# Performance work log

Measured on AMD Instinct MI355X. Metric: run time of the kernel, lower is better.

The kernel has to match this reference:

```python
import jax, jax.numpy as jnp
import numpy as np

H, DM, LQ, LK, DK, DV = 16, 1024, 2048, 2048, 64, 64
B = 2

def setup_inputs() -> dict:
    key = jax.random.key(0)
    ks = jax.random.split(key, 12)
    s = 0.02  # init scale for weights
    return {
        "Q": jax.random.normal(ks[0], (B, LQ, DM), jnp.float32),
        "K": jax.random.normal(ks[1], (B, LK, DM), jnp.float32),
        "V": jax.random.normal(ks[2], (B, LK, DM), jnp.float32),
        "mask": jax.random.randint(ks[3], (B, LQ), 0, 2, jnp.int32),
        "W_Q": jax.random.normal(ks[4], (H * DK, DM), jnp.float32) * s,
        "b_Q": jnp.zeros((H * DK,), jnp.float32),
        "W_K": jax.random.normal(ks[5], (H * DK, DM), jnp.float32) * s,
        "b_K": jnp.zeros((H * DK,), jnp.float32),
        "W_V": jax.random.normal(ks[6], (H * DV, DM), jnp.float32) * s,
        "b_V": jnp.zeros((H * DV,), jnp.float32),
        "W_O": jax.random.normal(ks[7], (DM, H * DV), jnp.float32) * s,
        "b_O": jnp.zeros((DM,), jnp.float32),
    }

def reference(Q, K, V, mask, W_Q, b_Q, W_K, b_K, W_V, b_V, W_O, b_O):
    b = Q.shape[0]
    q = (Q @ W_Q.T + b_Q).reshape(b, LQ, H, DK)
    k = (K @ W_K.T + b_K).reshape(b, LK, H, DK)
    v = (V @ W_V.T + b_V).reshape(b, LK, H, DV)
    # scores: [b, h, q, k]
    A = jnp.einsum('bqhd,bkhd->bhqk', q, k) / jnp.sqrt(jnp.float32(DK))
    # mask masks whole QUERY rows; softmax is over the query axis (dim=1 in torch's [B*h, lq, lk])
    A = jnp.where(mask[:, None, :, None] == 0, -jnp.inf, A)
    alpha = jax.nn.softmax(A, axis=2)  # over query axis, per original masked branch
    out = jnp.einsum('bhqk,bkhd->bqhd', alpha, v).reshape(b, LQ, H * DV)
    return out @ W_O.T + b_O + Q  # output proj + residual
```

## Files before the change

### kernel.cpp

```cpp
#include <hip/hip_runtime.h>
#include <hip/hip_bf16.h>
#include <stdint.h>

using frag8 = __attribute__((ext_vector_type(8))) short;
using f32x4 = __attribute__((ext_vector_type(4))) float;

#define MFMA16 __builtin_amdgcn_mfma_f32_16x16x32_bf16

#if __has_builtin(__builtin_amdgcn_exp2f)
#define EXP2F(x) __builtin_amdgcn_exp2f(x)
#else
#define EXP2F(x) __expf((x) * 0.6931471805599453f)
#endif
#if __has_builtin(__builtin_amdgcn_rcpf)
#define RCPF(x) __builtin_amdgcn_rcpf(x)
#else
#define RCPF(x) (1.0f / (x))
#endif

#define SCALE_Q 0.18033688011112042f

__device__ __forceinline__ short f2bf(float f) {
    union { __hip_bfloat16 h; short s; } c;
    c.h = __float2bfloat16(f);
    return c.s;
}
__device__ __forceinline__ float bf2f(short s) {
    union { uint32_t u; float f; } x; x.u = ((uint32_t)(uint16_t)s) << 16;
    return x.f;
}
__device__ __forceinline__ uint32_t pack2bf(float a, float b) {
    float2 t; t.x = a; t.y = b;
    __hip_bfloat162 h = __float22bfloat162_rn(t);
    union { __hip_bfloat162 h; uint32_t u; } c; c.h = h;
    return c.u;
}
__device__ __forceinline__ uint32_t addpk(uint32_t a, uint32_t b) {
    float a0 = bf2f((short)(a & 0xffff)), a1 = bf2f((short)(a >> 16));
    float b0 = bf2f((short)(b & 0xffff)), b1 = bf2f((short)(b >> 16));
    return pack2bf(a0 + b0, a1 + b1);
}
__device__ __forceinline__ frag8 add8(uint4 x, uint4 y) {
    union { uint32_t u[4]; frag8 f; } r;
    r.u[0] = addpk(x.x, y.x); r.u[1] = addpk(x.y, y.y);
    r.u[2] = addpk(x.z, y.z); r.u[3] = addpk(x.w, y.w);
    return r.f;
}

__global__ __launch_bounds__(64) void k_compact(const int* __restrict__ mask,
                                                int* __restrict__ idx,
                                                int* __restrict__ invp,
                                                int* __restrict__ nU) {
    const int b = blockIdx.x, ln = threadIdx.x;
    const int* m = mask + b * 2048;
    int tot = 0;
    for (int c = 0; c < 32; c++)
        tot += __popcll(__ballot(m[c * 64 + ln] != 0));
    int base = 0, mbase = tot;
    for (int c = 0; c < 32; c++) {
        int i = c * 64 + ln;
        int mv = m[i];
        unsigned long long bal = __ballot(mv != 0);
        int rank = __popcll(bal & ((1ull << ln) - 1ull));
        int nb = __popcll(bal);
        int pos = mv ? (base + rank) : (mbase + ln - rank);
        invp[b * 2048 + i] = pos;
        if (mv) idx[b * 2048 + pos] = i;
        base += nb; mbase += 64 - nb;
    }
    if (ln == 0) nU[b] = tot;
}

__global__ __launch_bounds__(256) void k_zero2(uint4* __restrict__ a,
                                               uint4* __restrict__ b, int n16) {
    int i = blockIdx.x * 256 + threadIdx.x;
    if (i < n16) { uint4 z = {0, 0, 0, 0}; a[i] = z; b[i] = z; }
}

__global__ __launch_bounds__(256) void k_cvt_all(
    const float* __restrict__ s0, const float* __restrict__ s1,
    const float* __restrict__ s2, const float* __restrict__ s3,
    const float* __restrict__ s4, const float* __restrict__ s5,
    const float* __restrict__ s6,
    short* __restrict__ d0, short* __restrict__ d1, short* __restrict__ d2,
    short* __restrict__ d3, short* __restrict__ d4, short* __restrict__ d5,
    short* __restrict__ d6) {
    const int A4 = 1048576, W4 = 262144;
    int i = blockIdx.x * 256 + threadIdx.x;
    int st = gridDim.x * 256;
    const int total = 3 * A4 + 4 * W4;
    for (; i < total; i += st) {
        const float* s; short* d; int j;
        if (i < A4)            { s = s0; d = d0; j = i; }
        else if (i < 2 * A4)   { s = s1; d = d1; j = i - A4; }
        else if (i < 3 * A4)   { s = s2; d = d2; j = i - 2 * A4; }
        else {
            int t = i - 3 * A4; int seg = t / W4; j = t - seg * W4;
            s = seg == 0 ? s3 : seg == 1 ? s4 : seg == 2 ? s5 : s6;
            d = seg == 0 ? d3 : seg == 1 ? d4 : seg == 2 ? d5 : d6;
        }
        float4 v = reinterpret_cast<const float4*>(s)[j];
        uint2 o;
        o.x = pack2bf(v.x, v.y);
        o.y = pack2bf(v.z, v.w);
        reinterpret_cast<uint2*>(d)[j] = o;
    }
}

__device__ __forceinline__ void stage64x128(const short* __restrict__ g, int rs,
                                            short* lds, int tid) {
#pragma unroll
    for (int j = 0; j < 2; j++) {
        int chunk = j * 256 + tid;
        int row = chunk >> 3, c = chunk & 7;
        int sc = c ^ (row & 7);
        __builtin_amdgcn_global_load_lds(
            (const __attribute__((address_space(1))) uint32_t*)(g + (size_t)row * rs + sc * 8),
            (__attribute__((address_space(3))) uint32_t*)(lds + (j * 256 + (tid & 192)) * 8),
            16, 0, 0);
    }
}
__device__ __forceinline__ frag8 ldswz(const short* lds, int row, int cc) {
    return *(const frag8*)(lds + row * 64 + ((cc ^ (row & 7)) << 3));
}

__device__ __forceinline__ void stage_gswz(const short* __restrict__ g,
                                           short* lds, int tid) {
#pragma unroll
    for (int j = 0; j < 2; j++) {
        int c = j * 256 + tid;
        int lrow = c >> 3;
        int sc = (c & 7) ^ (lrow & 7);
        int grow = lrow * 2 + (sc >> 2);
        int gcol = (sc & 3) * 8;
        __builtin_amdgcn_global_load_lds(
            (const __attribute__((address_space(1))) uint32_t*)(g + (size_t)grow * 1024 + gcol),
            (__attribute__((address_space(3))) uint32_t*)(lds + (j * 256 + (tid & 192)) * 8),
            16, 0, 0);
    }
}
__device__ __forceinline__ frag8 ldgswz(const short* lds, int row, int cc) {
    int lrow = row >> 1;
    int s = (((row & 1) << 2) + cc) ^ (lrow & 7);
    return *(const frag8*)(lds + lrow * 64 + s * 8);
}

__global__ __launch_bounds__(256) void k_proj3(
    const short* __restrict__ A0, const short* __restrict__ A1, const short* __restrict__ A2,
    const short* __restrict__ B0, const short* __restrict__ B1, const short* __restrict__ B2,
    const float* __restrict__ bias0, const float* __restrict__ bias1, const float* __restrict__ bias2,
    const int* __restrict__ invp,
    short* __restrict__ dst0, short* __restrict__ dst1, short* __restrict__ dst2) {
    __shared__ short lA[2][4096];
    __shared__ short lB[2][4096];
    const int wg = blockIdx.x;
    const int tmlow = wg & 7, tnb = (wg >> 3) & 7, rest = wg >> 6;
    const int tmh = rest & 3, z = rest >> 2;
    const int tmb = tmlow | (tmh << 3);
    const short* A  = z == 0 ? A0 : z == 1 ? A1 : A2;
    const short* Bt = z == 0 ? B0 : z == 1 ? B1 : B2;
    const float* bias = z == 0 ? bias0 : z == 1 ? bias1 : bias2;
    short* dst = z == 0 ? dst0 : z == 1 ? dst1 : dst2;
    const float scale = z == 0 ? SCALE_Q : 1.0f;

    const int tid = threadIdx.x, w = tid >> 6, ln = tid & 63;
    const int wm = w >> 1, wn = w & 1, r16 = ln & 15, g = ln >> 4;
    const int tn = tnb * 128, tm = tmb * 128;
    const short* Ab = A + (size_t)tm * 1024;
    const short* Bb = Bt + (size_t)tn * 1024;

    f32x4 acc[4][4] = {};
    stage_gswz(Ab, &lA[0][0], tid);
    stage_gswz(Bb, &lB[0][0], tid);
    int buf = 0;
    for (int ks = 0; ks < 32; ks++) {
        __syncthreads();
        if (ks + 1 < 32) {
            stage_gswz(Ab + (ks + 1) * 32, &lA[buf ^ 1][0], tid);
            stage_gswz(Bb + (ks + 1) * 32, &lB[buf ^ 1][0], tid);
        }
        frag8 af[4], bg[4];
#pragma unroll
        for (int mf = 0; mf < 4; mf++)
            af[mf] = ldgswz(&lA[buf][0], wm * 64 + mf * 16 + r16, g);
#pragma unroll
        for (int nf = 0; nf < 4; nf++)
            bg[nf] = ldgswz(&lB[buf][0], wn * 64 + nf * 16 + r16, g);
#pragma unroll
        for (int mf = 0; mf < 4; mf++)
#pragma unroll
            for (int nf = 0; nf < 4; nf++)
                acc[mf][nf] = MFMA16(af[mf], bg[nf], acc[mf][nf], 0, 0, 0);
        buf ^= 1;
    }
#pragma unroll
    for (int mf = 0; mf < 4; mf++)
#pragma unroll
        for (int r = 0; r < 4; r++) {
            int m = tm + wm * 64 + mf * 16 + g * 4 + r;
            int b = m >> 11, seq = m & 2047;
            int sq = (z == 0) ? invp[b * 2048 + seq] : seq;
#pragma unroll
            for (int nf = 0; nf < 4; nf++) {
                int n = tn + wn * 64 + nf * 16 + r16;
                float val = (acc[mf][nf][r] + bias[n]) * scale;
                int h = n >> 6, d = n & 63;
                dst[((size_t)(b * 16 + h) * 2048 + sq) * 64 + d] = f2bf(val);
            }
        }
}

__global__ __launch_bounds__(256, 3) void k_stats(const short* __restrict__ k_s,
                                                  const short* __restrict__ q_s,
                                                  const int* __restrict__ nU,
                                                  const short* __restrict__ v_s,
                                                  short* __restrict__ vhatT) {
    __shared__ short lQ[2][4096];
    __shared__ float lD[128];
    __shared__ short lT[128 * 70];
    const int wg = blockIdx.x;
    const int x = wg & 7, r2 = wg >> 3;
    const int kt = r2 & 15;
    const int bh = x + 8 * (r2 >> 4);
    const int b = bh >> 4;
    const int n = nU[b], nUr = (n + 63) & ~63;
    const int tid = threadIdx.x, w = tid >> 6, ln = tid & 63;
    const int r16 = ln & 15, g = ln >> 4;
    const int kbase = kt * 128 + w * 32;

    const short* kp = k_s + ((size_t)bh * 2048 + kbase) * 64;
    frag8 kf[2][2];
#pragma unroll
    for (int mfk = 0; mfk < 2; mfk++)
#pragma unroll
        for (int kk = 0; kk < 2; kk++)
            kf[mfk][kk] = *(const frag8*)(kp + (mfk * 16 + r16) * 64 + kk * 32 + g * 8);

    const short* qsp = q_s + (size_t)bh * 2048 * 64;
    float dacc[2][4] = {};
    const f32x4 z4 = {0.f, 0.f, 0.f, 0.f};

    if (nUr > 0) {
        stage64x128(qsp, 64, &lQ[0][0], tid);
        int buf = 0;
        for (int qb = 0; qb < nUr; qb += 64) {
            __syncthreads();
            if (qb + 64 < nUr)
                stage64x128(qsp + (size_t)(qb + 64) * 64, 64, &lQ[buf ^ 1][0], tid);
            const short* Qc = &lQ[buf][0];
#pragma unroll
            for (int nf = 0; nf < 4; nf++) {
                float fm = (qb + nf * 16 + r16 < n) ? 1.0f : 0.0f;
                frag8 bq0 = ldswz(Qc, nf * 16 + r16, g);
                frag8 bq1 = ldswz(Qc, nf * 16 + r16, 4 + g);
#pragma unroll
                for (int mfk = 0; mfk < 2; mfk++) {
                    f32x4 s = MFMA16(kf[mfk][0], bq0, z4, 0, 0, 0);
                    s = MFMA16(kf[mfk][1], bq1, s, 0, 0, 0);
#pragma unroll
                    for (int r = 0; r < 4; r++)
                        dacc[mfk][r] += fm * EXP2F(s[r]);
                }
            }
            buf ^= 1;
        }
    }
#pragma unroll
    for (int mfk = 0; mfk < 2; mfk++)
#pragma unroll
        for (int r = 0; r < 4; r++) {
            float v = dacc[mfk][r];
#pragma unroll
            for (int off = 1; off < 16; off <<= 1)
                v += __shfl_xor(v, off, 16);
            dacc[mfk][r] = v;
        }
    if (r16 == 0) {
#pragma unroll
        for (int mfk = 0; mfk < 2; mfk++)
#pragma unroll
            for (int r = 0; r < 4; r++)
                lD[w * 32 + mfk * 16 + g * 4 + r] = RCPF(dacc[mfk][r]);
    }
    const short* vrow = v_s + ((size_t)bh * 2048 + kt * 128) * 64;
#pragma unroll
    for (int i = 0; i < 8; i++) {
        int idx4 = i * 256 + tid;
        int row = idx4 >> 4, c4 = idx4 & 15;
        uint2 u = *(const uint2*)(vrow + (size_t)row * 64 + c4 * 4);
        *(uint32_t*)&lT[row * 70 + c4 * 4]     = u.x;
        *(uint32_t*)&lT[row * 70 + c4 * 4 + 2] = u.y;
    }
    __syncthreads();
    {
        int d = tid >> 2, kc = tid & 3;
        short* dstp = vhatT + ((size_t)bh * 64 + d) * 2048 + kt * 128 + kc * 32;
        uint32_t wd[16];
#pragma unroll
        for (int j2 = 0; j2 < 16; j2++) {
            int k0 = kc * 32 + j2 * 2;
            float v0 = bf2f(lT[k0 * 70 + d]) * lD[k0];
            float v1 = bf2f(lT[(k0 + 1) * 70 + d]) * lD[k0 + 1];
            wd[j2] = pack2bf(v0, v1);
        }
#pragma unroll
        for (int j4 = 0; j4 < 4; j4++) {
            uint4 o = {wd[j4 * 4], wd[j4 * 4 + 1], wd[j4 * 4 + 2], wd[j4 * 4 + 3]};
            *((uint4*)dstp + j4) = o;
        }
    }
}

__global__ __launch_bounds__(256, 3) void k_apply(const short* __restrict__ q_s,
                                                  const short* __restrict__ k_s,
                                                  const short* __restrict__ vhatT,
                                                  const int* __restrict__ idx,
                                                  const int* __restrict__ nU,
                                                  short* __restrict__ p0,
                                                  short* __restrict__ p1) {
    __shared__ short lK[2][4096];
    __shared__ short lV[2][4096];
    __shared__ short lP[128 * 64];
    const int wg = blockIdx.x;
    const int x = wg & 7, r2 = wg >> 3;
    const int qt = r2 & 15, y = r2 >> 4;
    const int bhsp = (y << 3) | x;
    const int bh = bhsp >> 1, sp = bhsp & 1;
    const int b = bh >> 4, h = bh & 15;
    const int n = nU[b];
    if (qt * 128 >= n) return;
    const int tid = threadIdx.x, w = tid >> 6, ln = tid & 63;
    const int r16 = ln & 15, g = ln >> 4;

    const short* qp = q_s + ((size_t)bh * 2048 + qt * 128 + w * 32) * 64;
    frag8 qf[2][2];
#pragma unroll
    for (int qi = 0; qi < 2; qi++)
#pragma unroll
        for (int kk = 0; kk < 2; kk++)
            qf[qi][kk] = *(const frag8*)(qp + (qi * 16 + r16) * 64 + kk * 32 + g * 8);

    const short* kp = k_s + ((size_t)bh * 2048 + sp * 1024) * 64;
    const short* vp = vhatT + (size_t)bh * 64 * 2048 + sp * 1024;

    f32x4 oacc[2][4] = {};
    const f32x4 z4 = {0.f, 0.f, 0.f, 0.f};

    stage64x128(kp, 64, &lK[0][0], tid);
    stage64x128(vp, 2048, &lV[0][0], tid);
    int buf = 0;
    for (int kb = 0; kb < 1024; kb += 64) {
        __syncthreads();
        if (kb + 64 < 1024) {
            stage64x128(kp + (size_t)(kb + 64) * 64, 64, &lK[buf ^ 1][0], tid);
            stage64x128(vp + kb + 64, 2048, &lV[buf ^ 1][0], tid);
        }
        const short* Kc = &lK[buf][0];
        const short* Vc = &lV[buf][0];
        frag8 vb[4][2];
#pragma unroll
        for (int nf = 0; nf < 4; nf++)
#pragma unroll
            for (int kk = 0; kk < 2; kk++)
                vb[nf][kk] = ldswz(Vc, nf * 16 + r16, kk * 4 + g);
#pragma unroll
        for (int qi = 0; qi < 2; qi++) {
            const int prow = w * 32 + qi * 16 + r16;
            const int rx = prow & 7;
#pragma unroll
            for (int mf2 = 0; mf2 < 4; mf2++) {
                f32x4 s = z4;
#pragma unroll
                for (int kk = 0; kk < 2; kk++)
                    s = MFMA16(ldswz(Kc, mf2 * 16 + r16, kk * 4 + g), qf[qi][kk], s, 0, 0, 0);
                float e0 = EXP2F(s[0]), e1 = EXP2F(s[1]);
                float e2 = EXP2F(s[2]), e3 = EXP2F(s[3]);
                uint2 pk;
                pk.x = pack2bf(e0, e1);
                pk.y = pack2bf(e2, e3);
                int o = mf2 * 32 + g * 8;
                int addr = prow * 128 + (((o >> 4) ^ rx) << 4) + (o & 15);
                *(uint2*)((char*)lP + addr) = pk;
            }
        }
#pragma unroll
        for (int qi = 0; qi < 2; qi++) {
            const int prow = w * 32 + qi * 16 + r16;
            const int rx = prow & 7;
            frag8 pa[2];
#pragma unroll
            for (int kk = 0; kk < 2; kk++)
                pa[kk] = *(const frag8*)((char*)lP + prow * 128 + (((kk * 4 + g) ^ rx) << 4));
#pragma unroll
            for (int nf = 0; nf < 4; nf++)
#pragma unroll
                for (int kk = 0; kk < 2; kk++)
                    oacc[qi][nf] = MFMA16(pa[kk], vb[nf][kk], oacc[qi][nf], 0, 0, 0);
        }
        buf ^= 1;
    }
    short* op = sp ? p1 : p0;
#pragma unroll
    for (int qi = 0; qi < 2; qi++)
#pragma unroll
        for (int r = 0; r < 4; r++) {
            int lq = qt * 128 + w * 32 + qi * 16 + g * 4 + r;
            if (lq < n) {
                int qg = idx[b * 2048 + lq];
#pragma unroll
                for (int nf = 0; nf < 4; nf++) {
                    int d = nf * 16 + r16;
                    op[((size_t)(b * 2048 + qg)) * 1024 + h * 64 + d] = f2bf(oacc[qi][nf][r]);
                }
            }
        }
}

__global__ __launch_bounds__(256) void k_final(const short* __restrict__ p0,
                                               const short* __restrict__ p1,
                                               const short* __restrict__ Bt,
                                               const float* __restrict__ bias,
                                               const float* __restrict__ Qres,
                                               float* __restrict__ out) {
    __shared__ short lA[2][4096];
    __shared__ short lB[2][4096];
    const int wg = blockIdx.x;
    const int tmb = (wg & 7) | ((wg >> 6) << 3);
    const int tnb = (wg >> 3) & 7;
    const int tid = threadIdx.x, w = tid >> 6, ln = tid & 63;
    const int wm = w >> 1, wn = w & 1, r16 = ln & 15, g = ln >> 4;
    const int tn = tnb * 128, tm = tmb * 128;
    const short* A0 = p0 + (size_t)tm * 1024;
    const short* A1 = p1 + (size_t)tm * 1024;
    const short* Bb = Bt + (size_t)tn * 1024;

    const int c0 = (w * 2) * 64 + ln, c1 = c0 + 64;
    const int lr0 = c0 >> 3, s0 = (c0 & 7) ^ (lr0 & 7);
    const int gr0 = lr0 * 2 + (s0 >> 2), gc0 = (s0 & 3) * 8;
    const int lr1 = c1 >> 3, s1 = (c1 & 7) ^ (lr1 & 7);
    const int gr1 = lr1 * 2 + (s1 >> 2), gc1 = (s1 & 3) * 8;

    f32x4 acc[4][4] = {};
    uint4 ra0, rb0, ra1, rb1;

    {
        uint4 x0 = *(const uint4*)(A0 + (size_t)gr0 * 1024 + gc0);
        uint4 y0 = *(const uint4*)(A1 + (size_t)gr0 * 1024 + gc0);
        uint4 x1 = *(const uint4*)(A0 + (size_t)gr1 * 1024 + gc1);
        uint4 y1 = *(const uint4*)(A1 + (size_t)gr1 * 1024 + gc1);
        stage_gswz(Bb, &lB[0][0], tid);
        *(frag8*)&lA[0][c0 * 8] = add8(x0, y0);
        *(frag8*)&lA[0][c1 * 8] = add8(x1, y1);
        ra0 = *(const uint4*)(A0 + (size_t)gr0 * 1024 + 32 + gc0);
        rb0 = *(const uint4*)(A1 + (size_t)gr0 * 1024 + 32 + gc0);
        ra1 = *(const uint4*)(A0 + (size_t)gr1 * 1024 + 32 + gc1);
        rb1 = *(const uint4*)(A1 + (size_t)gr1 * 1024 + 32 + gc1);
    }
    int buf = 0;
    for (int ks = 0; ks < 32; ks++) {
        __syncthreads();
        if (ks + 1 < 32) {
            *(frag8*)&lA[buf ^ 1][c0 * 8] = add8(ra0, rb0);
            *(frag8*)&lA[buf ^ 1][c1 * 8] = add8(ra1, rb1);
            stage_gswz(Bb + (ks + 1) * 32, &lB[buf ^ 1][0], tid);
        }
        if (ks + 2 < 32) {
            ra0 = *(const uint4*)(A0 + (size_t)gr0 * 1024 + (ks + 2) * 32 + gc0);
            rb0 = *(const uint4*)(A1 + (size_t)gr0 * 1024 + (ks + 2) * 32 + gc0);
            ra1 = *(const uint4*)(A0 + (size_t)gr1 * 1024 + (ks + 2) * 32 + gc1);
            rb1 = *(const uint4*)(A1 + (size_t)gr1 * 1024 + (ks + 2) * 32 + gc1);
        }
        frag8 af[4], bg[4];
#pragma unroll
        for (int mf = 0; mf < 4; mf++)
            af[mf] = ldgswz(&lA[buf][0], wm * 64 + mf * 16 + r16, g);
#pragma unroll
        for (int nf = 0; nf < 4; nf++)
            bg[nf] = ldgswz(&lB[buf][0], wn * 64 + nf * 16 + r16, g);
#pragma unroll
        for (int mf = 0; mf < 4; mf++)
#pragma unroll
            for (int nf = 0; nf < 4; nf++)
                acc[mf][nf] = MFMA16(af[mf], bg[nf], acc[mf][nf], 0, 0, 0);
        buf ^= 1;
    }
#pragma unroll
    for (int mf = 0; mf < 4; mf++)
#pragma unroll
        for (int nf = 0; nf < 4; nf++)
#pragma unroll
            for (int r = 0; r < 4; r++) {
                int m = tm + wm * 64 + mf * 16 + g * 4 + r;
                int n = tn + wn * 64 + nf * 16 + r16;
                float val = acc[mf][nf][r] + bias[n] + Qres[(size_t)m * 1024 + n];
                out[(size_t)m * 1024 + n] = val;
            }
}

extern "C" void kernel_launch(void* const* d_in, const int* in_sizes, int n_in,
                              void* d_out, int out_size, void* d_ws, size_t ws_size,
                              hipStream_t stream) {
    (void)in_sizes; (void)n_in; (void)out_size; (void)ws_size;
    const float* Qf  = (const float*)d_in[0];
    const float* Kf  = (const float*)d_in[1];
    const float* Vf  = (const float*)d_in[2];
    const int*   msk = (const int*)d_in[3];
    const float* WQ  = (const float*)d_in[4];
    const float* bQ  = (const float*)d_in[5];
    const float* WK  = (const float*)d_in[6];
    const float* bK  = (const float*)d_in[7];
    const float* WV  = (const float*)d_in[8];
    const float* bV  = (const float*)d_in[9];
    const float* WO  = (const float*)d_in[10];
    const float* bO  = (const float*)d_in[11];
    float* out = (float*)d_out;

    char* p = (char*)d_ws;
    const size_t SZ_ACT = (size_t)4096 * 1024 * 2;
    const size_t SZ_W   = (size_t)1024 * 1024 * 2;
    short* Qb  = (short*)p; p += SZ_ACT;
    short* Kb  = (short*)p; p += SZ_ACT;
    short* Vb  = (short*)p; p += SZ_ACT;
    short* q_s = (short*)p; p += SZ_ACT;
    short* k_s = (short*)p; p += SZ_ACT;
    short* v_s = (short*)p; p += SZ_ACT;
    short* Wqb = (short*)p; p += SZ_W;
    short* Wkb = (short*)p; p += SZ_W;
    short* Wvb = (short*)p; p += SZ_W;
    short* Wob = (short*)p; p += SZ_W;
    int* idx  = (int*)p; p += (size_t)2 * 2048 * 4;
    int* invp = (int*)p; p += (size_t)2 * 2048 * 4;
    int* nU   = (int*)p; p += 256;
    short* vhatT = Qb;
    short* p0    = Kb;
    short* p1    = Vb;

    k_compact<<<2, 64, 0, stream>>>(msk, idx, invp, nU);

    k_cvt_all<<<4096, 256, 0, stream>>>(Qf, Kf, Vf, WQ, WK, WV, WO,
                                        Qb, Kb, Vb, Wqb, Wkb, Wvb, Wob);

    k_proj3<<<768, 256, 0, stream>>>(Qb, Kb, Vb, Wqb, Wkb, Wvb,
                                     bQ, bK, bV, invp, q_s, k_s, v_s);

    k_stats<<<512, 256, 0, stream>>>(k_s, q_s, nU, v_s, vhatT);

    k_zero2<<<2048, 256, 0, stream>>>((uint4*)p0, (uint4*)p1, 524288);

    k_apply<<<1024, 256, 0, stream>>>(q_s, k_s, vhatT, idx, nU, p0, p1);

    k_final<<<256, 256, 0, stream>>>(p0, p1, Wob, bO, Qf, out);
}
```

Measured before the change: 161.3 us.

## Pre-sum partial outputs in separate kernel and shrink final GEMM N-tile to 64

A new k_psum kernel adds the two bf16 partial attention outputs p0 and p1 before the output projection. k_final can then stage A straight into LDS with global_load_lds, dropping the register round-trip and in-loop add it used before. The final GEMM tile goes from 128x128 to 128x64, so the grid doubles from 256 to 512 blocks for better occupancy and CU coverage across the device. The cost is an extra kernel launch and an extra read and write pass over the partial buffers, plus more re-reads of A across the wider N grid.

```diff
diff --git a/kernel.cpp b/kernel.cpp
--- a/kernel.cpp
+++ b/kernel.cpp
@@ -75,6 +75,18 @@
                                                uint4* __restrict__ b, int n16) {
     int i = blockIdx.x * 256 + threadIdx.x;
     if (i < n16) { uint4 z = {0, 0, 0, 0}; a[i] = z; b[i] = z; }
+}
+
+__global__ __launch_bounds__(256) void k_psum(short* __restrict__ p0,
+                                              const short* __restrict__ p1, int n8) {
+    int i = blockIdx.x * 256 + threadIdx.x;
+    int st = gridDim.x * 256;
+    for (; i < n8; i += st) {
+        uint4 a = ((const uint4*)p0)[i];
+        uint4 b = ((const uint4*)p1)[i];
+        frag8 r = add8(a, b);
+        ((uint4*)p0)[i] = *(uint4*)&r;
+    }
 }
 
 __global__ __launch_bounds__(256) void k_cvt_all(
@@ -139,6 +151,18 @@
             16, 0, 0);
     }
 }
+__device__ __forceinline__ void stage_gswz64(const short* __restrict__ g,
+                                             short* lds, int tid) {
+    int c = tid;
+    int lrow = c >> 3;
+    int sc = (c & 7) ^ (lrow & 7);
+    int grow = lrow * 2 + (sc >> 2);
+    int gcol = (sc & 3) * 8;
+    __builtin_amdgcn_global_load_lds(
+        (const __attribute__((address_space(1))) uint32_t*)(g + (size_t)grow * 1024 + gcol),
+        (__attribute__((address_space(3))) uint32_t*)(lds + (tid & 192) * 8),
+        16, 0, 0);
+}
 __device__ __forceinline__ frag8 ldgswz(const short* lds, int row, int cc) {
     int lrow = row >> 1;
     int s = (((row & 1) << 2) + cc) ^ (lrow & 7);
@@ -416,82 +440,55 @@
         }
 }
 
-__global__ __launch_bounds__(256) void k_final(const short* __restrict__ p0,
-                                               const short* __restrict__ p1,
+__global__ __launch_bounds__(256) void k_final(const short* __restrict__ A,
                                                const short* __restrict__ Bt,
                                                const float* __restrict__ bias,
                                                const float* __restrict__ Qres,
                                                float* __restrict__ out) {
     __shared__ short lA[2][4096];
-    __shared__ short lB[2][4096];
+    __shared__ short lB[2][2048];
     const int wg = blockIdx.x;
-    const int tmb = (wg & 7) | ((wg >> 6) << 3);
-    const int tnb = (wg >> 3) & 7;
+    const int x = wg & 7, r2 = wg >> 3;
+    const int tnb = r2 & 15, tmh = r2 >> 4;
+    const int tmb = x | (tmh << 3);
     const int tid = threadIdx.x, w = tid >> 6, ln = tid & 63;
     const int wm = w >> 1, wn = w & 1, r16 = ln & 15, g = ln >> 4;
-    const int tn = tnb * 128, tm = tmb * 128;
-    const short* A0 = p0 + (size_t)tm * 1024;
-    const short* A1 = p1 + (size_t)tm * 1024;
+    const int tn = tnb * 64, tm = tmb * 128;
+    const short* Ab = A + (size_t)tm * 1024;
     const short* Bb = Bt + (size_t)tn * 1024;
 
-    const int c0 = (w * 2) * 64 + ln, c1 = c0 + 64;
-    const int lr0 = c0 >> 3, s0 = (c0 & 7) ^ (lr0 & 7);
-    const int gr0 = lr0 * 2 + (s0 >> 2), gc0 = (s0 & 3) * 8;
-    const int lr1 = c1 >> 3, s1 = (c1 & 7) ^ (lr1 & 7);
-    const int gr1 = lr1 * 2 + (s1 >> 2), gc1 = (s1 & 3) * 8;
-
-    f32x4 acc[4][4] = {};
-    uint4 ra0, rb0, ra1, rb1;
-
-    {
-        uint4 x0 = *(const uint4*)(A0 + (size_t)gr0 * 1024 + gc0);
-        uint4 y0 = *(const uint4*)(A1 + (size_t)gr0 * 1024 + gc0);
-        uint4 x1 = *(const uint4*)(A0 + (size_t)gr1 * 1024 + gc1);
-        uint4 y1 = *(const uint4*)(A1 + (size_t)gr1 * 1024 + gc1);
-        stage_gswz(Bb, &lB[0][0], tid);
-        *(frag8*)&lA[0][c0 * 8] = add8(x0, y0);
-        *(frag8*)&lA[0][c1 * 8] = add8(x1, y1);
-        ra0 = *(const uint4*)(A0 + (size_t)gr0 * 1024 + 32 + gc0);
-        rb0 = *(const uint4*)(A1 + (size_t)gr0 * 1024 + 32 + gc0);
-        ra1 = *(const uint4*)(A0 + (size_t)gr1 * 1024 + 32 + gc1);
-        rb1 = *(const uint4*)(A1 + (size_t)gr1 * 1024 + 32 + gc1);
-    }
+    f32x4 acc[4][2] = {};
+    stage_gswz(Ab, &lA[0][0], tid);
+    stage_gswz64(Bb, &lB[0][0], tid);
     int buf = 0;
     for (int ks = 0; ks < 32; ks++) {
         __syncthreads();
         if (ks + 1 < 32) {
-            *(frag8*)&lA[buf ^ 1][c0 * 8] = add8(ra0, rb0);
-            *(frag8*)&lA[buf ^ 1][c1 * 8] = add8(ra1, rb1);
-            stage_gswz(Bb + (ks + 1) * 32, &lB[buf ^ 1][0], tid);
-        }
-        if (ks + 2 < 32) {
-            ra0 = *(const uint4*)(A0 + (size_t)gr0 * 1024 + (ks + 2) * 32 + gc0);
-            rb0 = *(const uint4*)(A1 + (size_t)gr0 * 1024 + (ks + 2) * 32 + gc0);
-            ra1 = *(const uint4*)(A0 + (size_t)gr1 * 1024 + (ks + 2) * 32 + gc1);
-            rb1 = *(const uint4*)(A1 + (size_t)gr1 * 1024 + (ks + 2) * 32 + gc1);
-        }
-        frag8 af[4], bg[4];
+            stage_gswz(Ab + (ks + 1) * 32, &lA[buf ^ 1][0], tid);
+            stage_gswz64(Bb + (ks + 1) * 32, &lB[buf ^ 1][0], tid);
+        }
+        frag8 af[4], bg[2];
 #pragma unroll
         for (int mf = 0; mf < 4; mf++)
             af[mf] = ldgswz(&lA[buf][0], wm * 64 + mf * 16 + r16, g);
 #pragma unroll
-        for (int nf = 0; nf < 4; nf++)
-            bg[nf] = ldgswz(&lB[buf][0], wn * 64 + nf * 16 + r16, g);
+        for (int nf = 0; nf < 2; nf++)
+            bg[nf] = ldgswz(&lB[buf][0], wn * 32 + nf * 16 + r16, g);
 #pragma unroll
         for (int mf = 0; mf < 4; mf++)
 #pragma unroll
-            for (int nf = 0; nf < 4; nf++)
+            for (int nf = 0; nf < 2; nf++)
                 acc[mf][nf] = MFMA16(af[mf], bg[nf], acc[mf][nf], 0, 0, 0);
         buf ^= 1;
     }
 #pragma unroll
     for (int mf = 0; mf < 4; mf++)
 #pragma unroll
-        for (int nf = 0; nf < 4; nf++)
+        for (int nf = 0; nf < 2; nf++)
 #pragma unroll
             for (int r = 0; r < 4; r++) {
                 int m = tm + wm * 64 + mf * 16 + g * 4 + r;
-                int n = tn + wn * 64 + nf * 16 + r16;
+                int n = tn + wn * 32 + nf * 16 + r16;
                 float val = acc[mf][nf][r] + bias[n] + Qres[(size_t)m * 1024 + n];
                 out[(size_t)m * 1024 + n] = val;
             }
@@ -549,5 +546,7 @@
 
     k_apply<<<1024, 256, 0, stream>>>(q_s, k_s, vhatT, idx, nU, p0, p1);
 
-    k_final<<<256, 256, 0, stream>>>(p0, p1, Wob, bO, Qf, out);
-}
+    k_psum<<<2048, 256, 0, stream>>>(p0, p1, 524288);
+
+    k_final<<<512, 256, 0, stream>>>(p0, Wob, bO, Qf, out);
+}
```

Result: faster. 157.9 us (-2.1%).
